# Kernel optimization log

Measured on AMD Instinct MI355X. Metric: run time of the kernel, lower is better.

The kernel has to match this reference:

```python
import jax, jax.numpy as jnp
import numpy as np
import math

B, L, H, E = 16, 1024, 8, 64   # L = nsensor = N (forced by einsum 'bhls,bhlg')
WIN = 1024                      # win_size, last dim of x
G = 64                          # n_group
D_SEL = 1                       # d_sel default


def setup_inputs() -> dict:
    key = jax.random.key(0)
    ks = jax.random.split(key, 7)
    return {
        "queries": jax.random.normal(ks[0], (B, L, H, E), dtype=jnp.float32),
        "keys": jax.random.normal(ks[1], (B, L, H, E), dtype=jnp.float32),
        "values": jax.random.normal(ks[2], (B, L, H, E), dtype=jnp.float32),
        "x": jax.random.normal(ks[3], (B, L, WIN), dtype=jnp.float32),
        "mlp_w": jax.random.normal(ks[4], (H * D_SEL, WIN), dtype=jnp.float32) * 0.02,
        "mlp_b": jax.random.normal(ks[5], (H * D_SEL,), dtype=jnp.float32) * 0.02,
        "sel_W": jax.random.normal(ks[6], (H, G, D_SEL), dtype=jnp.float32),
        "attn_mask": 0,
    }


def _select_attention(x, mlp_w, mlp_b, sel_W, n_heads, d_sel):
    b, n, lwin = x.shape
    xf = x.reshape(b * n, lwin)
    newx = jnp.tanh(xf @ mlp_w.T + mlp_b)                 # [(B*N), H*d_sel]
    # Faithful raw reshape (torch.reshape, no permute): mixes n and h axes.
    newx = newx.reshape(b, n_heads, n, d_sel)             # [B, H, N, d_sel]
    sel = jnp.einsum('bhnd,hgd->bhng', newx, sel_W)       # [B, H, N, G]
    return jax.nn.relu(sel)


def reference(queries, keys, values, x, mlp_w, mlp_b, sel_W, attn_mask):
    b, l, h, e = queries.shape
    scale = 1.0 / math.sqrt(e)
    scores = jnp.einsum('blhe,bshe->bhls', queries, keys)      # [B, H, L, S]
    sel = _select_attention(x, mlp_w, mlp_b, sel_W, h, D_SEL)  # [B, H, L, G]
    scores = jnp.einsum('bhls,bhlg->bhsg', scores, sel)        # [B, H, S, G]
    series = jax.nn.softmax(scale * scores, axis=-1)           # softmax over groups
    # values labeled 'blhs': l=S (value len), s=D (feature). Output V: [B, D, H, G]
    V = jnp.einsum('blhs,bhlg->bshg', values, series)
    return V
```

## Files before the change

kernel.cpp:

```cpp
#include <hip/hip_runtime.h>
#include <math.h>

#define NB 16
#define NL 1024
#define NH 8
#define NE 64
#define NWIN 1024
#define NG 64

#define SCH 128
#define SROW 136

typedef __attribute__((ext_vector_type(8))) short short8;
typedef __attribute__((ext_vector_type(4))) float floatx4;

__device__ __forceinline__ short f2bf(float x) {
    unsigned u = __float_as_uint(x);
    u += 0x7fffu + ((u >> 16) & 1u);
    return (short)(u >> 16);
}
__device__ __forceinline__ float dot4(float4 a, float4 b) {
    return fmaf(a.x, b.x, fmaf(a.y, b.y, fmaf(a.z, b.z, a.w * b.w)));
}

__global__ __launch_bounds__(256) void k_sel_q(
    const float* __restrict__ x, const float* __restrict__ mlp_w,
    const float* __restrict__ mlp_b, const float* __restrict__ q,
    float* __restrict__ qp, float* __restrict__ qn)
{
    __shared__ float4 w_lds[8][NWIN / 4];
    __shared__ float t_lds[256];
    __shared__ float redp[4][64], redn[4][64];

    int tid = threadIdx.x;
    int blk = blockIdx.x;
    int qq = blk & 3, bh = blk >> 2;
    int b = bh >> 3, h = bh & 7;
    int w = tid >> 6, lane = tid & 63;

    const float4* w4 = (const float4*)mlp_w;
    float4* wl = (float4*)w_lds;
    #pragma unroll
    for (int i = 0; i < 8; ++i)
        wl[tid + 256 * i] = w4[tid + 256 * i];
    __syncthreads();

    float4 keep03 = make_float4(0,0,0,0), keep47 = make_float4(0,0,0,0);
    int r0 = b * 1024 + h * 128 + qq * 32 + w * 8;
    for (int j = 0; j < 8; ++j) {
        const float4* xr = (const float4*)(x + (size_t)(r0 + j) * NWIN);
        float4 a03 = make_float4(0,0,0,0), a47 = make_float4(0,0,0,0);
        #pragma unroll
        for (int it = 0; it < 4; ++it) {
            float4 xv = xr[it * 64 + lane];
            a03.x += dot4(xv, w_lds[0][it * 64 + lane]);
            a03.y += dot4(xv, w_lds[1][it * 64 + lane]);
            a03.z += dot4(xv, w_lds[2][it * 64 + lane]);
            a03.w += dot4(xv, w_lds[3][it * 64 + lane]);
            a47.x += dot4(xv, w_lds[4][it * 64 + lane]);
            a47.y += dot4(xv, w_lds[5][it * 64 + lane]);
            a47.z += dot4(xv, w_lds[6][it * 64 + lane]);
            a47.w += dot4(xv, w_lds[7][it * 64 + lane]);
        }
        #pragma unroll
        for (int off = 1; off < 64; off <<= 1) {
            a03.x += __shfl_xor(a03.x, off, 64);
            a03.y += __shfl_xor(a03.y, off, 64);
            a03.z += __shfl_xor(a03.z, off, 64);
            a03.w += __shfl_xor(a03.w, off, 64);
            a47.x += __shfl_xor(a47.x, off, 64);
            a47.y += __shfl_xor(a47.y, off, 64);
            a47.z += __shfl_xor(a47.z, off, 64);
            a47.w += __shfl_xor(a47.w, off, 64);
        }
        if (lane == j) { keep03 = a03; keep47 = a47; }
    }
    if (lane < 8) {
        float4 b03 = *(const float4*)mlp_b;
        float4 b47 = *(const float4*)(mlp_b + 4);
        float4 t03, t47;
        t03.x = tanhf(keep03.x + b03.x); t03.y = tanhf(keep03.y + b03.y);
        t03.z = tanhf(keep03.z + b03.z); t03.w = tanhf(keep03.w + b03.w);
        t47.x = tanhf(keep47.x + b47.x); t47.y = tanhf(keep47.y + b47.y);
        t47.z = tanhf(keep47.z + b47.z); t47.w = tanhf(keep47.w + b47.w);
        *(float4*)&t_lds[w * 64 + lane * 8]     = t03;
        *(float4*)&t_lds[w * 64 + lane * 8 + 4] = t47;
    }
    __syncthreads();

    int lo = lane >> 4, e4 = lane & 15;
    float4 accp = make_float4(0,0,0,0), accn = make_float4(0,0,0,0);
    #pragma unroll 4
    for (int i = 0; i < 16; ++i) {
        int l_loc = w * 64 + i * 4 + lo;
        float tv = t_lds[l_loc];
        int l = qq * 256 + l_loc;
        float4 qv = *(const float4*)(q + (((size_t)(b * NL + l)) * NH + h) * NE + e4 * 4);
        float tp = fmaxf(tv, 0.f), tn = fminf(tv, 0.f);
        accp.x = fmaf(tp, qv.x, accp.x); accp.y = fmaf(tp, qv.y, accp.y);
        accp.z = fmaf(tp, qv.z, accp.z); accp.w = fmaf(tp, qv.w, accp.w);
        accn.x = fmaf(tn, qv.x, accn.x); accn.y = fmaf(tn, qv.y, accn.y);
        accn.z = fmaf(tn, qv.z, accn.z); accn.w = fmaf(tn, qv.w, accn.w);
    }
    #pragma unroll
    for (int off = 16; off <= 32; off <<= 1) {
        accp.x += __shfl_xor(accp.x, off, 64); accp.y += __shfl_xor(accp.y, off, 64);
        accp.z += __shfl_xor(accp.z, off, 64); accp.w += __shfl_xor(accp.w, off, 64);
        accn.x += __shfl_xor(accn.x, off, 64); accn.y += __shfl_xor(accn.y, off, 64);
        accn.z += __shfl_xor(accn.z, off, 64); accn.w += __shfl_xor(accn.w, off, 64);
    }
    if (lo == 0) {
        *(float4*)&redp[w][e4 * 4] = accp;
        *(float4*)&redn[w][e4 * 4] = accn;
    }
    __syncthreads();
    if (tid < 64) {
        atomicAdd(&qp[bh * NE + tid], redp[0][tid] + redp[1][tid] + redp[2][tid] + redp[3][tid]);
    } else if (tid < 128) {
        int e = tid - 64;
        atomicAdd(&qn[bh * NE + e], redn[0][e] + redn[1][e] + redn[2][e] + redn[3][e]);
    }
}

__global__ __launch_bounds__(256, 4) void k_attn_out(
    const float* __restrict__ keys, const float* __restrict__ values,
    const float* __restrict__ sel_W,
    const float* __restrict__ qp, const float* __restrict__ qn,
    float* __restrict__ out)
{
    __shared__ short sb[NG][SROW];
    __shared__ float ap_l[SCH], an_l[SCH];
    __shared__ float2 wpn[NG];
    __shared__ float mx2[2][SCH], dn2[2][SCH];

    int tid = threadIdx.x, blk = blockIdx.x;
    int chunk = blk & 7, bh = blk >> 3;
    int b = bh >> 3, h = bh & 7;
    int w = tid >> 6, lane = tid & 63;
    int c = lane & 15, sq = lane >> 4;
    const float scale = 0.125f;

    if (tid < NG) {
        float W = sel_W[h * NG + tid];
        wpn[tid] = make_float2(fmaxf(W, 0.f) * scale, fminf(W, 0.f) * scale);
    }

    const float4 qp4 = *(const float4*)(qp + bh * NE + c * 4);
    const float4 qn4 = *(const float4*)(qn + bh * NE + c * 4);
    int s0 = chunk * SCH;

    #pragma unroll
    for (int p = 0; p < 8; ++p) {
        int sl = w * 32 + p * 4 + sq;
        float4 kv = *(const float4*)(keys + (((size_t)(b * NL + s0 + sl)) * NH + h) * NE + c * 4);
        float pp = dot4(kv, qp4);
        float pn = dot4(kv, qn4);
        #pragma unroll
        for (int m_ = 1; m_ <= 8; m_ <<= 1) {
            pp += __shfl_xor(pp, m_, 64);
            pn += __shfl_xor(pn, m_, 64);
        }
        if (c == 0) { ap_l[sl] = pp; an_l[sl] = pn; }
    }
    __syncthreads();

    {
        int s_ = tid & 127, gh = tid >> 7, g0 = gh * 32;
        float ap = ap_l[s_], an = an_l[s_];
        float m = -1e30f;
        #pragma unroll 8
        for (int g = 0; g < 32; ++g) {
            float2 wv = wpn[g0 + g];
            m = fmaxf(m, fmaf(wv.x, ap, wv.y * an));
        }
        mx2[gh][s_] = m;
        __syncthreads();
        m = fmaxf(mx2[0][s_], mx2[1][s_]);
        float d = 0.f;
        #pragma unroll 8
        for (int g = 0; g < 32; ++g) {
            float2 wv = wpn[g0 + g];
            d += __expf(fmaf(wv.x, ap, wv.y * an) - m);
        }
        dn2[gh][s_] = d;
        __syncthreads();
        float inv = 1.0f / (dn2[0][s_] + dn2[1][s_]);
        #pragma unroll 8
        for (int g = 0; g < 32; ++g) {
            float2 wv = wpn[g0 + g];
            sb[g0 + g][s_] = f2bf(__expf(fmaf(wv.x, ap, wv.y * an) - m) * inv);
        }
    }
    __syncthreads();

    floatx4 acc[4] = {{0.f,0.f,0.f,0.f},{0.f,0.f,0.f,0.f},
                      {0.f,0.f,0.f,0.f},{0.f,0.f,0.f,0.f}};
    const float* vbase = values + (((size_t)(b * NL + s0)) * NH + h) * NE + 16 * w + c;
    #pragma unroll
    for (int ks = 0; ks < 4; ++ks) {
        float a[8];
        #pragma unroll
        for (int j = 0; j < 8; ++j)
            a[j] = vbase[(size_t)(ks * 32 + sq * 8 + j) * (NH * NE)];
        short8 av;
        #pragma unroll
        for (int j = 0; j < 8; ++j) av[j] = f2bf(a[j]);
        #pragma unroll
        for (int n = 0; n < 4; ++n) {
            short8 bv = *(const short8*)&sb[16 * n + c][ks * 32 + sq * 8];
            acc[n] = __builtin_amdgcn_mfma_f32_16x16x32_bf16(av, bv, acc[n], 0, 0, 0);
        }
    }

    #pragma unroll
    for (int n = 0; n < 4; ++n) {
        #pragma unroll
        for (int r = 0; r < 4; ++r) {
            int e = 16 * w + sq * 4 + r;
            int g = 16 * n + c;
            atomicAdd(&out[((size_t)(b * NE + e) * NH + h) * NG + g], acc[n][r]);
        }
    }
}

extern "C" void kernel_launch(void* const* d_in, const int* in_sizes, int n_in,
                              void* d_out, int out_size, void* d_ws, size_t ws_size,
                              hipStream_t stream) {
    (void)in_sizes; (void)n_in; (void)ws_size;
    const float* queries = (const float*)d_in[0];
    const float* keys    = (const float*)d_in[1];
    const float* values  = (const float*)d_in[2];
    const float* x       = (const float*)d_in[3];
    const float* mlp_w   = (const float*)d_in[4];
    const float* mlp_b   = (const float*)d_in[5];
    const float* sel_W   = (const float*)d_in[6];
    float* out = (float*)d_out;

    float* qp_ws = (float*)d_ws;
    float* qn_ws = qp_ws + NB * NH * NE;

    hipMemsetAsync(out, 0, (size_t)out_size * sizeof(float), stream);
    hipMemsetAsync(qp_ws, 0, (size_t)2 * NB * NH * NE * sizeof(float), stream);

    k_sel_q<<<dim3(NB * NH * 4), dim3(256), 0, stream>>>(x, mlp_w, mlp_b,
                                                          queries, qp_ws, qn_ws);
    k_attn_out<<<dim3(NB * NH * 8), dim3(256), 0, stream>>>(keys, values, sel_W,
                                                            qp_ws, qn_ws, out);
}
```

Before: 197.6 us.

## Split sel_q work across twice as many blocks with 16-lane row reductions

Doubles the k_sel_q grid so each block handles 16 x rows (128 query positions) instead of 32 rows (256 positions). Each wave now computes four rows at once, one per 16-lane group, which shortens the shuffle reduction from six steps to four and drops the serial per-row loop and lane-select. It also adds an occupancy hint to the launch bounds. The aim is more parallelism and less reduction overhead in the MLP/tanh stage, at the cost of loading the 32KB weight tile into LDS twice as many times overall.

```diff
diff --git a/kernel.cpp b/kernel.cpp
--- a/kernel.cpp
+++ b/kernel.cpp
@@ -23,20 +23,21 @@
     return fmaf(a.x, b.x, fmaf(a.y, b.y, fmaf(a.z, b.z, a.w * b.w)));
 }
 
-__global__ __launch_bounds__(256) void k_sel_q(
+__global__ __launch_bounds__(256, 4) void k_sel_q(
     const float* __restrict__ x, const float* __restrict__ mlp_w,
     const float* __restrict__ mlp_b, const float* __restrict__ q,
     float* __restrict__ qp, float* __restrict__ qn)
 {
     __shared__ float4 w_lds[8][NWIN / 4];
-    __shared__ float t_lds[256];
+    __shared__ float t_lds[128];
     __shared__ float redp[4][64], redn[4][64];
 
     int tid = threadIdx.x;
     int blk = blockIdx.x;
-    int qq = blk & 3, bh = blk >> 2;
+    int ee = blk & 7, bh = blk >> 3;
     int b = bh >> 3, h = bh & 7;
     int w = tid >> 6, lane = tid & 63;
+    int sq = lane >> 4, c = lane & 15;
 
     const float4* w4 = (const float4*)mlp_w;
     float4* wl = (float4*)w_lds;
@@ -45,56 +46,53 @@
         wl[tid + 256 * i] = w4[tid + 256 * i];
     __syncthreads();
 
-    float4 keep03 = make_float4(0,0,0,0), keep47 = make_float4(0,0,0,0);
-    int r0 = b * 1024 + h * 128 + qq * 32 + w * 8;
-    for (int j = 0; j < 8; ++j) {
-        const float4* xr = (const float4*)(x + (size_t)(r0 + j) * NWIN);
-        float4 a03 = make_float4(0,0,0,0), a47 = make_float4(0,0,0,0);
-        #pragma unroll
-        for (int it = 0; it < 4; ++it) {
-            float4 xv = xr[it * 64 + lane];
-            a03.x += dot4(xv, w_lds[0][it * 64 + lane]);
-            a03.y += dot4(xv, w_lds[1][it * 64 + lane]);
-            a03.z += dot4(xv, w_lds[2][it * 64 + lane]);
-            a03.w += dot4(xv, w_lds[3][it * 64 + lane]);
-            a47.x += dot4(xv, w_lds[4][it * 64 + lane]);
-            a47.y += dot4(xv, w_lds[5][it * 64 + lane]);
-            a47.z += dot4(xv, w_lds[6][it * 64 + lane]);
-            a47.w += dot4(xv, w_lds[7][it * 64 + lane]);
-        }
-        #pragma unroll
-        for (int off = 1; off < 64; off <<= 1) {
-            a03.x += __shfl_xor(a03.x, off, 64);
-            a03.y += __shfl_xor(a03.y, off, 64);
-            a03.z += __shfl_xor(a03.z, off, 64);
-            a03.w += __shfl_xor(a03.w, off, 64);
-            a47.x += __shfl_xor(a47.x, off, 64);
-            a47.y += __shfl_xor(a47.y, off, 64);
-            a47.z += __shfl_xor(a47.z, off, 64);
-            a47.w += __shfl_xor(a47.w, off, 64);
-        }
-        if (lane == j) { keep03 = a03; keep47 = a47; }
-    }
-    if (lane < 8) {
+    int row_loc = w * 4 + sq;
+    int r = b * 1024 + h * 128 + ee * 16 + row_loc;
+    const float4* xr = (const float4*)(x + (size_t)r * NWIN);
+    float4 a03 = make_float4(0,0,0,0), a47 = make_float4(0,0,0,0);
+    #pragma unroll
+    for (int i = 0; i < 16; ++i) {
+        float4 xv = xr[i * 16 + c];
+        a03.x += dot4(xv, w_lds[0][i * 16 + c]);
+        a03.y += dot4(xv, w_lds[1][i * 16 + c]);
+        a03.z += dot4(xv, w_lds[2][i * 16 + c]);
+        a03.w += dot4(xv, w_lds[3][i * 16 + c]);
+        a47.x += dot4(xv, w_lds[4][i * 16 + c]);
+        a47.y += dot4(xv, w_lds[5][i * 16 + c]);
+        a47.z += dot4(xv, w_lds[6][i * 16 + c]);
+        a47.w += dot4(xv, w_lds[7][i * 16 + c]);
+    }
+    #pragma unroll
+    for (int off = 1; off < 16; off <<= 1) {
+        a03.x += __shfl_xor(a03.x, off, 64);
+        a03.y += __shfl_xor(a03.y, off, 64);
+        a03.z += __shfl_xor(a03.z, off, 64);
+        a03.w += __shfl_xor(a03.w, off, 64);
+        a47.x += __shfl_xor(a47.x, off, 64);
+        a47.y += __shfl_xor(a47.y, off, 64);
+        a47.z += __shfl_xor(a47.z, off, 64);
+        a47.w += __shfl_xor(a47.w, off, 64);
+    }
+    if (c == 0) {
         float4 b03 = *(const float4*)mlp_b;
         float4 b47 = *(const float4*)(mlp_b + 4);
         float4 t03, t47;
-        t03.x = tanhf(keep03.x + b03.x); t03.y = tanhf(keep03.y + b03.y);
-        t03.z = tanhf(keep03.z + b03.z); t03.w = tanhf(keep03.w + b03.w);
-        t47.x = tanhf(keep47.x + b47.x); t47.y = tanhf(keep47.y + b47.y);
-        t47.z = tanhf(keep47.z + b47.z); t47.w = tanhf(keep47.w + b47.w);
-        *(float4*)&t_lds[w * 64 + lane * 8]     = t03;
-        *(float4*)&t_lds[w * 64 + lane * 8 + 4] = t47;
-    }
-    __syncthreads();
-
-    int lo = lane >> 4, e4 = lane & 15;
+        t03.x = tanhf(a03.x + b03.x); t03.y = tanhf(a03.y + b03.y);
+        t03.z = tanhf(a03.z + b03.z); t03.w = tanhf(a03.w + b03.w);
+        t47.x = tanhf(a47.x + b47.x); t47.y = tanhf(a47.y + b47.y);
+        t47.z = tanhf(a47.z + b47.z); t47.w = tanhf(a47.w + b47.w);
+        *(float4*)&t_lds[row_loc * 8]     = t03;
+        *(float4*)&t_lds[row_loc * 8 + 4] = t47;
+    }
+    __syncthreads();
+
+    int lo = sq, e4 = c;
     float4 accp = make_float4(0,0,0,0), accn = make_float4(0,0,0,0);
-    #pragma unroll 4
-    for (int i = 0; i < 16; ++i) {
-        int l_loc = w * 64 + i * 4 + lo;
+    #pragma unroll
+    for (int i = 0; i < 8; ++i) {
+        int l_loc = w * 32 + i * 4 + lo;
         float tv = t_lds[l_loc];
-        int l = qq * 256 + l_loc;
+        int l = ee * 128 + l_loc;
         float4 qv = *(const float4*)(q + (((size_t)(b * NL + l)) * NH + h) * NE + e4 * 4);
         float tp = fmaxf(tv, 0.f), tn = fminf(tv, 0.f);
         accp.x = fmaf(tp, qv.x, accp.x); accp.y = fmaf(tp, qv.y, accp.y);
@@ -242,7 +240,7 @@
     hipMemsetAsync(out, 0, (size_t)out_size * sizeof(float), stream);
     hipMemsetAsync(qp_ws, 0, (size_t)2 * NB * NH * NE * sizeof(float), stream);
 
-    k_sel_q<<<dim3(NB * NH * 4), dim3(256), 0, stream>>>(x, mlp_w, mlp_b,
+    k_sel_q<<<dim3(NB * NH * 8), dim3(256), 0, stream>>>(x, mlp_w, mlp_b,
                                                           queries, qp_ws, qn_ws);
     k_attn_out<<<dim3(NB * NH * 8), dim3(256), 0, stream>>>(keys, values, sel_W,
                                                             qp_ws, qn_ws, out);
```

New measurement: 203.2 us. 1.03x slower.
